# Optimization experiments

Hardware: AMD Instinct MI355X
Metric: run time of the kernel (lower is better)

The kernel has to match this reference:

```python
import jax, jax.numpy as jnp
import numpy as np

B, S, H, NH, BLK, R = 2, 4096, 768, 12, 64, 3
D = H // NH
NB = S // BLK
PENALTY = -10000.0


def setup_inputs() -> dict:
    key = jax.random.key(0)
    ks = jax.random.split(key, 5)
    return {
        "hidden_states": jax.random.normal(ks[0], (B, S, H), dtype=jnp.float32),
        "Wq": jax.random.normal(ks[1], (H, H), dtype=jnp.float32) * 0.02,
        "Wk": jax.random.normal(ks[2], (H, H), dtype=jnp.float32) * 0.02,
        "Wv": jax.random.normal(ks[3], (H, H), dtype=jnp.float32) * 0.02,
        "band_mask": jnp.ones((B, 1, NB - 4, BLK, 3 * BLK), dtype=jnp.float32),
        "from_mask": jnp.ones((B, 1, S, 1), dtype=jnp.float32),
        "to_mask": jnp.ones((B, 1, 1, S), dtype=jnp.float32),
        "from_blocked_mask": jnp.ones((B, NB, BLK), dtype=jnp.float32),
        "to_blocked_mask": jnp.ones((B, NB, BLK), dtype=jnp.float32),
        "rand_attn": jax.random.randint(ks[4], (B, NH, NB - 2, R), 0, NB, dtype=jnp.int64),
    }


def reference(hidden_states, Wq, Wk, Wv, band_mask, from_mask, to_mask,
              from_blocked_mask, to_blocked_mask, rand_attn):
    b, s, _ = hidden_states.shape
    nb, blk, r = NB, BLK, R
    rsqrt_d = 1.0 / jnp.sqrt(jnp.float32(D))
    sm = jax.nn.softmax

    # projections -> [b, h, s, d]
    def proj(W):
        return jnp.einsum('bse,ed->bsd', hidden_states, W).reshape(b, s, NH, D).transpose(0, 2, 1, 3)
    q, k, v = proj(Wq), proj(Wk), proj(Wv)

    bq = q.reshape(b, NH, nb, blk, D)
    bk = k.reshape(b, NH, nb, blk, D)
    bv = v.reshape(b, NH, nb, blk, D)

    # gather random key/value blocks: [b, h, nb-2, r*blk, d]
    bi = jnp.arange(b)[:, None, None, None]
    hi = jnp.arange(NH)[None, :, None, None]
    gk = bk[bi, hi, rand_attn].reshape(b, NH, nb - 2, r * blk, D)
    gv = bv[bi, hi, rand_attn].reshape(b, NH, nb - 2, r * blk, D)

    # random mask: [b, h, nb-2, blk, r*blk]
    rm = to_blocked_mask[jnp.arange(b)[:, None, None, None], rand_attn]  # [b,h,nb-2,r,blk]
    rm = rm.reshape(b, NH, nb - 2, r * blk)
    rand_mask = jnp.einsum('blq,bhlk->bhlqk', from_blocked_mask[:, 1:-1], rm)

    ones_rand = jnp.ones((b, 1, 1, r * blk), dtype=to_mask.dtype)
    ones_4blk = jnp.ones((b, NH, blk, 4 * blk), dtype=rand_mask.dtype)

    # --- first (global) block: attends to everything ---
    fp = jnp.einsum('bhqd,bhkd->bhqk', bq[:, :, 0], k) * rsqrt_d + (1.0 - to_mask) * PENALTY
    fc = jnp.einsum('bhqk,bhkd->bhqd', sm(fp, axis=-1), v)[:, :, None]  # [b,h,1,blk,d]

    # --- second block: first 3 blocks + last block + random blocks ---
    sk = jnp.concatenate([bk[:, :, 0], bk[:, :, 1], bk[:, :, 2], bk[:, :, -1], gk[:, :, 0]], axis=2)
    sv = jnp.concatenate([bv[:, :, 0], bv[:, :, 1], bv[:, :, 2], bv[:, :, -1], gv[:, :, 0]], axis=2)
    sp = jnp.einsum('bhqd,bhkd->bhqk', bq[:, :, 1], sk) * rsqrt_d
    seq_pad = jnp.concatenate([to_mask[:, :, :, :3 * blk], to_mask[:, :, :, -blk:], ones_rand], axis=3)
    rand_pad = jnp.concatenate([ones_4blk, rand_mask[:, :, 0]], axis=3)
    sp = sp + (1.0 - jnp.minimum(seq_pad, rand_pad)) * PENALTY
    sc = jnp.einsum('bhqk,bhkd->bhqd', sm(sp, axis=-1), sv)[:, :, None]

    # --- middle blocks: sliding window + global first/last + random ---
    ek = jnp.concatenate([bk[:, :, 1:-3], bk[:, :, 2:-2], bk[:, :, 3:-1]], axis=3)  # [b,h,nb-4,3blk,d]
    ev = jnp.concatenate([bv[:, :, 1:-3], bv[:, :, 2:-2], bv[:, :, 3:-1]], axis=3)
    mq = bq[:, :, 2:-2]
    inner = jnp.einsum('bhlqd,bhlkd->bhlqk', mq, ek) * rsqrt_d + (1.0 - band_mask) * PENALTY
    randb = jnp.einsum('bhlqd,bhlkd->bhlqk', mq, gk[:, :, 1:-1]) * rsqrt_d + (1.0 - rand_mask[:, :, 1:-1]) * PENALTY
    firstb = jnp.einsum('bhlqd,bhkd->bhlqk', mq, bk[:, :, 0]) * rsqrt_d + (1.0 - to_mask[:, :, :, None, :blk]) * PENALTY
    lastb = jnp.einsum('bhlqd,bhkd->bhlqk', mq, bk[:, :, -1]) * rsqrt_d + (1.0 - to_mask[:, :, :, None, -blk:]) * PENALTY
    band = jnp.concatenate([firstb, inner, randb, lastb], axis=-1)  # [...,(5+r)*blk]
    aw = sm(band, axis=-1)
    ctx_mid = (jnp.einsum('bhlqk,bhlkd->bhlqd', aw[..., blk:4 * blk], ev)
               + jnp.einsum('bhlqk,bhlkd->bhlqd', aw[..., 4 * blk:-blk], gv[:, :, 1:-1])
               + jnp.einsum('bhlqk,bhkd->bhlqd', aw[..., :blk], bv[:, :, 0])
               + jnp.einsum('bhlqk,bhkd->bhlqd', aw[..., -blk:], bv[:, :, -1]))

    # --- second-last block ---
    slk = jnp.concatenate([bk[:, :, 0], bk[:, :, -3], bk[:, :, -2], bk[:, :, -1], gk[:, :, -1]], axis=2)
    slv = jnp.concatenate([bv[:, :, 0], bv[:, :, -3], bv[:, :, -2], bv[:, :, -1], gv[:, :, -1]], axis=2)
    slp = jnp.einsum('bhqd,bhkd->bhqk', bq[:, :, -2], slk) * rsqrt_d
    sl_seq_pad = jnp.concatenate([to_mask[:, :, :, :blk], to_mask[:, :, :, -3 * blk:], ones_rand], axis=3)
    sl_rand_pad = jnp.concatenate([ones_4blk, rand_mask[:, :, -1]], axis=3)
    slp = slp + (1.0 - jnp.minimum(sl_seq_pad, sl_rand_pad)) * PENALTY
    slc = jnp.einsum('bhqk,bhkd->bhqd', sm(slp, axis=-1), slv)[:, :, None]

    # --- last (global) block ---
    lp = jnp.einsum('bhqd,bhkd->bhqk', bq[:, :, -1], k) * rsqrt_d + (1.0 - to_mask) * PENALTY
    lc = jnp.einsum('bhqk,bhkd->bhqd', sm(lp, axis=-1), v)[:, :, None]

    ctx = jnp.concatenate([fc, sc, ctx_mid, slc, lc], axis=2).reshape(b, NH, s, D)
    ctx = ctx * from_mask  # [b,1,s,1] broadcast
    return ctx.transpose(0, 2, 1, 3).reshape(b, s, NH * D)
```

## Files before the change

kernel.cpp:

```cpp
#include <hip/hip_runtime.h>
#include <hip/hip_bf16.h>
#include <stdint.h>

#define NHD 12
#define SLEN 4096
#define DH 64
#define NBLK 64
#define HDIM 768
#define PEN -10000.0f

typedef __bf16 bf16x8 __attribute__((ext_vector_type(8)));
typedef float f32x4 __attribute__((ext_vector_type(4)));
typedef unsigned short u16x8 __attribute__((ext_vector_type(8)));

__device__ __forceinline__ unsigned short f2bf(float x) {
    union { float f; unsigned u; } v; v.f = x;
    unsigned r = v.u + 0x7fffu + ((v.u >> 16) & 1u);
    return (unsigned short)(r >> 16);
}

__device__ __forceinline__ void gl2lds16(const void* g, void* l) {
    __builtin_amdgcn_global_load_lds(
        (const __attribute__((address_space(1))) void*)g,
        (__attribute__((address_space(3))) void*)l, 16, 0, 0);
}

__global__ void k_cast_hs(const float* __restrict__ in, unsigned short* __restrict__ out, int n8) {
    int i = blockIdx.x * blockDim.x + threadIdx.x;
    if (i >= n8) return;
    const float4* p = (const float4*)in + (size_t)i * 2;
    float4 a = p[0], b = p[1];
    u16x8 o;
    o[0]=f2bf(a.x); o[1]=f2bf(a.y); o[2]=f2bf(a.z); o[3]=f2bf(a.w);
    o[4]=f2bf(b.x); o[5]=f2bf(b.y); o[6]=f2bf(b.z); o[7]=f2bf(b.w);
    ((u16x8*)out)[i] = o;
}

__global__ void k_wt(const float* __restrict__ Wq, const float* __restrict__ Wk,
                     const float* __restrict__ Wv, unsigned short* __restrict__ wt) {
    const float* W = blockIdx.z == 0 ? Wq : (blockIdx.z == 1 ? Wk : Wv);
    unsigned short* out = wt + (size_t)blockIdx.z * HDIM * HDIM;
    __shared__ float tile[64][65];
    int t = threadIdx.x;
    int k0 = blockIdx.x * 64, n0 = blockIdx.y * 64;
    int r = t >> 2, c4 = t & 3;
#pragma unroll
    for (int j = 0; j < 16; j += 4) {
        float4 v = *(const float4*)&W[(size_t)(k0 + r) * HDIM + n0 + c4 * 16 + j];
        tile[r][c4*16+j+0] = v.x; tile[r][c4*16+j+1] = v.y;
        tile[r][c4*16+j+2] = v.z; tile[r][c4*16+j+3] = v.w;
    }
    __syncthreads();
    u16x8 o0, o1;
#pragma unroll
    for (int j = 0; j < 8; ++j) o0[j] = f2bf(tile[c4*16 + j][r]);
#pragma unroll
    for (int j = 0; j < 8; ++j) o1[j] = f2bf(tile[c4*16 + 8 + j][r]);
    *(u16x8*)&out[(size_t)(n0 + r) * HDIM + k0 + c4*16]     = o0;
    *(u16x8*)&out[(size_t)(n0 + r) * HDIM + k0 + c4*16 + 8] = o1;
}

__global__ __launch_bounds__(256) void k_proj(const unsigned short* __restrict__ hsb,
                                              const unsigned short* __restrict__ wtb,
                                              unsigned short* __restrict__ qkv) {
    __shared__ unsigned short As[128][72];
    __shared__ unsigned short Bs[128][72];
    const unsigned short* Bw = wtb + (size_t)blockIdx.z * HDIM * HDIM;
    unsigned short* out = qkv + (size_t)blockIdx.z * (2u * NHD * SLEN * DH);
    int m0 = blockIdx.x * 128, n0 = blockIdx.y * 128;
    int t = threadIdx.x;
    int w = t >> 6, l = t & 63, g = l >> 4, c = l & 15;
    int wm = w >> 1, wn = w & 1;
    int sr = t >> 1, sh = (t & 1) * 32;
    f32x4 acc[4][4];
#pragma unroll
    for (int i = 0; i < 4; ++i)
#pragma unroll
        for (int j = 0; j < 4; ++j) acc[i][j] = (f32x4){0.f,0.f,0.f,0.f};

    for (int kt = 0; kt < HDIM; kt += 64) {
        __syncthreads();
#pragma unroll
        for (int j = 0; j < 4; ++j) {
            *(u16x8*)&As[sr][sh + 8*j] = *(const u16x8*)&hsb[(size_t)(m0 + sr) * HDIM + kt + sh + 8*j];
            *(u16x8*)&Bs[sr][sh + 8*j] = *(const u16x8*)&Bw[(size_t)(n0 + sr) * HDIM + kt + sh + 8*j];
        }
        __syncthreads();
#pragma unroll
        for (int ks = 0; ks < 2; ++ks) {
            bf16x8 af[4], bf_[4];
#pragma unroll
            for (int mt = 0; mt < 4; ++mt) af[mt]  = *(const bf16x8*)&As[64*wm + 16*mt + c][32*ks + 8*g];
#pragma unroll
            for (int nt = 0; nt < 4; ++nt) bf_[nt] = *(const bf16x8*)&Bs[64*wn + 16*nt + c][32*ks + 8*g];
#pragma unroll
            for (int mt = 0; mt < 4; ++mt)
#pragma unroll
                for (int nt = 0; nt < 4; ++nt)
                    acc[mt][nt] = __builtin_amdgcn_mfma_f32_16x16x32_bf16(af[mt], bf_[nt], acc[mt][nt], 0, 0, 0);
        }
    }
#pragma unroll
    for (int mt = 0; mt < 4; ++mt)
#pragma unroll
        for (int nt = 0; nt < 4; ++nt)
#pragma unroll
            for (int r2 = 0; r2 < 4; ++r2) {
                int m = m0 + 64*wm + 16*mt + 4*g + r2;
                int n = n0 + 64*wn + 16*nt + c;
                int bb = m >> 12, s = m & 4095;
                int hh = n >> 6,  d = n & 63;
                out[(((size_t)bb * NHD + hh) * SLEN + s) * DH + d] = f2bf(acc[mt][nt][r2]);
            }
}

__global__ void k_vtrans(const unsigned short* __restrict__ v, unsigned short* __restrict__ vt) {
    __shared__ unsigned tile[64][65];
    int bh = blockIdx.y;
    int s0 = blockIdx.x * 64;
    int t = threadIdx.x;
    int r = t >> 2, c4 = t & 3;
    const unsigned short* vb = v + (size_t)bh * SLEN * DH;
#pragma unroll
    for (int jj = 0; jj < 16; jj += 8) {
        u16x8 x = *(const u16x8*)&vb[(size_t)(s0 + r) * DH + c4*16 + jj];
#pragma unroll
        for (int e = 0; e < 8; ++e) tile[r][c4*16 + jj + e] = x[e];
    }
    __syncthreads();
    unsigned short* vto = vt + (size_t)bh * DH * SLEN;
    int d = t >> 2;
    u16x8 o0, o1;
#pragma unroll
    for (int j = 0; j < 8; ++j) o0[j] = (unsigned short)tile[c4*16 + j][d];
#pragma unroll
    for (int j = 0; j < 8; ++j) o1[j] = (unsigned short)tile[c4*16 + 8 + j][d];
    *(u16x8*)&vto[(size_t)d * SLEN + s0 + c4*16]     = o0;
    *(u16x8*)&vto[(size_t)d * SLEN + s0 + c4*16 + 8] = o1;
}

__global__ __launch_bounds__(256) void k_attn(
    const unsigned short* __restrict__ Qb, const unsigned short* __restrict__ Kb,
    const unsigned short* __restrict__ VTb,
    const int* __restrict__ rand_attn,
    const float* __restrict__ band_mask, const float* __restrict__ from_mask,
    const float* __restrict__ to_mask, const float* __restrict__ fbm,
    const float* __restrict__ tbm,
    float* __restrict__ out, float* __restrict__ partials)
{
    __shared__ __align__(16) unsigned short Kt[2][4096];
    __shared__ __align__(16) unsigned short Vt[2][4096];
    __shared__ __align__(16) char plds[4 * 2048];

    int i0 = blockIdx.x;
    int gid = (i0 & 7) * 234 + (i0 >> 3);
    int bh = gid / 78, task = gid - bh * 78;
    int b = bh / NHD, h = bh - b * NHD;
    int t = threadIdx.x;
    int wq = t >> 6, l = t & 63, g = l >> 4, c = l & 15;
    int lr = l >> 3, ls = l & 7, sw = ls ^ lr;

    int row, mode = 0, pslot = 0;
    int blkj[8], kvj[8], sbj[8];
#pragma unroll
    for (int j = 0; j < 8; ++j) sbj[j] = 0;
    if (task < 8) {
        row = 0; mode = 1; pslot = task;
#pragma unroll
        for (int j = 0; j < 8; ++j) { blkj[j] = task * 8 + j; kvj[j] = 0; }
    } else if (task >= 70) {
        row = 63; mode = 1; pslot = task - 70;
#pragma unroll
        for (int j = 0; j < 8; ++j) { blkj[j] = pslot * 8 + j; kvj[j] = 0; }
    } else {
        row = task - 7;
        int rbase = ((b * NHD + h) * 62 + (row - 1)) * 3;
        blkj[4] = rand_attn[rbase];
        blkj[5] = rand_attn[rbase + 1];
        blkj[6] = rand_attn[rbase + 2];
        kvj[4] = kvj[5] = kvj[6] = 2;
        blkj[0] = 0; kvj[0] = 0;
        if (row == 1) {
            blkj[1]=1;  blkj[2]=2;  blkj[3]=63; kvj[1]=kvj[2]=kvj[3]=0;
            blkj[7]=0;  kvj[7]=3;
        } else if (row == 62) {
            blkj[1]=61; blkj[2]=62; blkj[3]=63; kvj[1]=kvj[2]=kvj[3]=0;
            blkj[7]=0;  kvj[7]=3;
        } else {
            blkj[1]=row-1; blkj[2]=row; blkj[3]=row+1;
            kvj[1]=kvj[2]=kvj[3]=1; sbj[1]=0; sbj[2]=64; sbj[3]=128;
            blkj[7]=63; kvj[7]=0;
        }
    }

    size_t bhoff = (size_t)bh * SLEN * DH;
    const char* Kbase = (const char*)(Kb + bhoff);
    const char* Vbase = (const char*)(VTb + (size_t)bh * DH * SLEN);
    int q0 = row * 64 + wq * 16;

    bf16x8 qf[2];
#pragma unroll
    for (int kk = 0; kk < 2; ++kk)
        qf[kk] = *(const bf16x8*)&Qb[bhoff + (size_t)(q0 + c) * DH + kk * 32 + 8 * g];

    float fmq = fbm[(b * NBLK + row) * 64 + wq * 16 + c];
    size_t bm_base = ((size_t)(b * 60 + row - 2) * 64 + (wq * 16 + c)) * 192;
    int tm_base = b * SLEN;

    float m_run = -1e30f, l_run = 0.f;
    f32x4 o_acc[4];
#pragma unroll
    for (int dt = 0; dt < 4; ++dt) o_acc[dt] = (f32x4){0.f,0.f,0.f,0.f};

    char* myl = plds + wq * 2048 + c * 128;
    int swz = (c & 7) << 4;

    auto stage = [&](int blk, int nb) __attribute__((always_inline)) {
#pragma unroll
        for (int ii = 0; ii < 2; ++ii) {
            int i = wq * 2 + ii;
            const char* ksrc = Kbase + (size_t)blk * 8192 + (size_t)(i*8 + lr) * 128 + sw * 16;
            gl2lds16(ksrc, (char*)&Kt[nb][0] + i * 1024);
            const char* vsrc = Vbase + (size_t)(i*8 + lr) * 8192 + (size_t)blk * 128 + sw * 16;
            gl2lds16(vsrc, (char*)&Vt[nb][0] + i * 1024);
        }
    };

    auto loadmask = [&](int kv, int blk, int sb, float4* mk) __attribute__((always_inline)) {
        if (kv == 0) {
#pragma unroll
            for (int mt = 0; mt < 4; ++mt)
                mk[mt] = *(const float4*)&to_mask[tm_base + blk * 64 + mt * 16 + 4 * g];
        } else if (kv == 1) {
#pragma unroll
            for (int mt = 0; mt < 4; ++mt)
                mk[mt] = *(const float4*)&band_mask[bm_base + sb + mt * 16 + 4 * g];
        } else if (kv == 2) {
#pragma unroll
            for (int mt = 0; mt < 4; ++mt)
                mk[mt] = *(const float4*)&tbm[(size_t)(b * NBLK + blk) * 64 + mt * 16 + 4 * g];
        }
    };

    auto compute = [&](int kv, int nb, const float4* mk) __attribute__((always_inline)) {
        if (kv == 3) return;
        int c7 = c & 7;
        bf16x8 kf[4][2];
#pragma unroll
        for (int mt = 0; mt < 4; ++mt)
#pragma unroll
            for (int kk = 0; kk < 2; ++kk)
                kf[mt][kk] = *(const bf16x8*)((const char*)&Kt[nb][0]
                              + (mt*16 + c) * 128 + (((kk*4 + g) ^ c7) * 16));

        f32x4 sa[4];
#pragma unroll
        for (int mt = 0; mt < 4; ++mt) sa[mt] = (f32x4){0.f,0.f,0.f,0.f};
#pragma unroll
        for (int kk = 0; kk < 2; ++kk)
#pragma unroll
            for (int mt = 0; mt < 4; ++mt)
                sa[mt] = __builtin_amdgcn_mfma_f32_16x16x32_bf16(kf[mt][kk], qf[kk], sa[mt], 0, 0, 0);

        float fmk = (kv == 2) ? fmq : 1.f;
#pragma unroll
        for (int mt = 0; mt < 4; ++mt) {
            sa[mt][0] = sa[mt][0] * 0.125f + (1.f - fmk * mk[mt].x) * PEN;
            sa[mt][1] = sa[mt][1] * 0.125f + (1.f - fmk * mk[mt].y) * PEN;
            sa[mt][2] = sa[mt][2] * 0.125f + (1.f - fmk * mk[mt].z) * PEN;
            sa[mt][3] = sa[mt][3] * 0.125f + (1.f - fmk * mk[mt].w) * PEN;
        }

        float pm = -1e30f;
#pragma unroll
        for (int mt = 0; mt < 4; ++mt)
#pragma unroll
            for (int r2 = 0; r2 < 4; ++r2) pm = fmaxf(pm, sa[mt][r2]);
        pm = fmaxf(pm, __shfl_xor(pm, 16));
        pm = fmaxf(pm, __shfl_xor(pm, 32));
        bool need = pm > m_run + 8.f;
        float mnew = need ? pm : m_run;
        float scale = __expf(m_run - mnew);
        m_run = mnew;
        l_run *= scale;
#pragma unroll
        for (int dt = 0; dt < 4; ++dt)
#pragma unroll
            for (int r2 = 0; r2 < 4; ++r2) o_acc[dt][r2] *= scale;

        float rs = 0.f;
#pragma unroll
        for (int mt = 0; mt < 4; ++mt)
#pragma unroll
            for (int r2 = 0; r2 < 4; ++r2) {
                float e = __expf(sa[mt][r2] - m_run);
                sa[mt][r2] = e;
                rs += e;
            }
        rs += __shfl_xor(rs, 16);
        rs += __shfl_xor(rs, 32);
        l_run += rs;

#pragma unroll
        for (int mt = 0; mt < 4; ++mt) {
            unsigned lo = (unsigned)f2bf(sa[mt][0]) | ((unsigned)f2bf(sa[mt][1]) << 16);
            unsigned hi = (unsigned)f2bf(sa[mt][2]) | ((unsigned)f2bf(sa[mt][3]) << 16);
            unsigned long long pk = (unsigned long long)lo | ((unsigned long long)hi << 32);
            *(unsigned long long*)(myl + ((mt * 32 + g * 8) ^ swz)) = pk;
        }
        asm volatile("" ::: "memory");
        bf16x8 pf0 = *(const bf16x8*)(myl + ((g * 16) ^ swz));
        bf16x8 pf1 = *(const bf16x8*)(myl + ((64 + g * 16) ^ swz));

#pragma unroll
        for (int dt = 0; dt < 4; ++dt) {
            bf16x8 v0 = *(const bf16x8*)((const char*)&Vt[nb][0]
                          + (dt*16 + c) * 128 + ((g ^ c7) * 16));
            bf16x8 v1 = *(const bf16x8*)((const char*)&Vt[nb][0]
                          + (dt*16 + c) * 128 + (((4 + g) ^ c7) * 16));
            o_acc[dt] = __builtin_amdgcn_mfma_f32_16x16x32_bf16(v0, pf0, o_acc[dt], 0, 0, 0);
            o_acc[dt] = __builtin_amdgcn_mfma_f32_16x16x32_bf16(v1, pf1, o_acc[dt], 0, 0, 0);
        }
    };

    float4 mkA[4], mkB[4];
    stage(blkj[0], 0);
    loadmask(kvj[0], blkj[0], sbj[0], mkA);
    __syncthreads();
#pragma unroll
    for (int tt = 0; tt < 8; ++tt) {
        if (tt < 7) {
            stage(blkj[tt + 1], (tt & 1) ^ 1);
            loadmask(kvj[tt + 1], blkj[tt + 1], sbj[tt + 1], (tt & 1) ? mkA : mkB);
        }
        compute(kvj[tt], tt & 1, (tt & 1) ? mkB : mkA);
        __syncthreads();
    }

    if (mode == 0) {
        int s = q0 + c;
        float fm = from_mask[b * SLEN + s];
        float inv = fm / l_run;
        size_t obase = ((size_t)b * SLEN + s) * HDIM + h * DH;
#pragma unroll
        for (int dt = 0; dt < 4; ++dt) {
            float4 val;
            val.x = o_acc[dt][0] * inv;
            val.y = o_acc[dt][1] * inv;
            val.z = o_acc[dt][2] * inv;
            val.w = o_acc[dt][3] * inv;
            *(float4*)&out[obase + dt * 16 + 4 * g] = val;
        }
    } else {
        float* pb = partials + (size_t)((bh * 2 + (row == 63 ? 1 : 0)) * 8 + pslot) * 4224;
        int q = wq * 16 + c;
#pragma unroll
        for (int dt = 0; dt < 4; ++dt) {
            float4 val;
            val.x = o_acc[dt][0]; val.y = o_acc[dt][1];
            val.z = o_acc[dt][2]; val.w = o_acc[dt][3];
            *(float4*)&pb[q * 64 + dt * 16 + 4 * g] = val;
        }
        if (g == 0) {
            pb[4096 + q] = m_run;
            pb[4160 + q] = l_run;
        }
    }
}

__global__ void k_combine(const float* __restrict__ partials, const float* __restrict__ from_mask,
                          float* __restrict__ out) {
    int gid = blockIdx.x;
    int bh = gid >> 1, rb = gid & 1;
    int b = bh / NHD, h = bh - b * NHD;
    int t = threadIdx.x;
    int q = t >> 2, dc = (t & 3) * 16;
    const float* base = partials + (size_t)gid * 8 * 4224;
    float M = -1e30f;
#pragma unroll
    for (int i = 0; i < 8; ++i) M = fmaxf(M, base[i*4224 + 4096 + q]);
    float L = 0.f, cx[16];
#pragma unroll
    for (int j = 0; j < 16; ++j) cx[j] = 0.f;
    for (int i = 0; i < 8; ++i) {
        float w = __expf(base[i*4224 + 4096 + q] - M);
        L += base[i*4224 + 4160 + q] * w;
#pragma unroll
        for (int j = 0; j < 16; ++j) cx[j] += base[i*4224 + q*64 + dc + j] * w;
    }
    int s = (rb ? 4032 : 0) + q;
    float fm = from_mask[b * SLEN + s];
    float inv = fm / L;
#pragma unroll
    for (int j = 0; j < 16; ++j)
        out[((size_t)b * SLEN + s) * HDIM + h * DH + dc + j] = cx[j] * inv;
}

extern "C" void kernel_launch(void* const* d_in, const int* in_sizes, int n_in,
                              void* d_out, int out_size, void* d_ws, size_t ws_size,
                              hipStream_t stream) {
    const float* hs    = (const float*)d_in[0];
    const float* Wq    = (const float*)d_in[1];
    const float* Wk    = (const float*)d_in[2];
    const float* Wv    = (const float*)d_in[3];
    const float* band  = (const float*)d_in[4];
    const float* fromm = (const float*)d_in[5];
    const float* tom   = (const float*)d_in[6];
    const float* fbm   = (const float*)d_in[7];
    const float* tbm   = (const float*)d_in[8];
    const int*   ra    = (const int*)d_in[9];
    float* out = (float*)d_out;

    char* ws = (char*)d_ws;
    unsigned short* hsb = (unsigned short*)(ws);
    unsigned short* vtb = (unsigned short*)(ws);
    unsigned short* wtb = (unsigned short*)(ws + 12582912);
    unsigned short* qkv = (unsigned short*)(ws + 16121856);
    float* partials     = (float*)(ws + 53870592);

    k_cast_hs<<<3072, 256, 0, stream>>>(hs, hsb, 786432);
    k_wt<<<dim3(12, 12, 3), 256, 0, stream>>>(Wq, Wk, Wv, wtb);
    k_proj<<<dim3(64, 6, 3), 256, 0, stream>>>(hsb, wtb, qkv);
    k_vtrans<<<dim3(64, 24), 256, 0, stream>>>(qkv + 2 * 6291456, vtb);
    k_attn<<<1872, 256, 0, stream>>>(qkv, qkv + 6291456, vtb, ra,
                                     band, fromm, tom, fbm, tbm, out, partials);
    k_combine<<<48, 256, 0, stream>>>(partials, fromm, out);
}
```

Measured before the change: 117.9 us.

## Fuse V transpose into projection, use async LDS loads, exp2 softmax with skip

The projection GEMM now loads tiles straight into swizzled LDS with global_load_lds. A transposed variant writes V directly in [d][s] layout, which removes the separate vtrans kernel and its round trip through memory. Attention folds log2e into the scale and precomputes the mask penalties during prefetch. It uses exp2f and skips the output rescale when no lane's running max changes, and converts to bf16 with native casts. The extra launch and the transposed scattered stores add cost in exchange.

```diff
diff --git a/kernel.cpp b/kernel.cpp
--- a/kernel.cpp
+++ b/kernel.cpp
@@ -8,6 +8,7 @@
 #define NBLK 64
 #define HDIM 768
 #define PEN -10000.0f
+#define LOG2E 1.44269504f
 
 typedef __bf16 bf16x8 __attribute__((ext_vector_type(8)));
 typedef float f32x4 __attribute__((ext_vector_type(4)));
@@ -60,18 +61,21 @@
     *(u16x8*)&out[(size_t)(n0 + r) * HDIM + k0 + c4*16 + 8] = o1;
 }
 
+template<bool TR>
 __global__ __launch_bounds__(256) void k_proj(const unsigned short* __restrict__ hsb,
                                               const unsigned short* __restrict__ wtb,
-                                              unsigned short* __restrict__ qkv) {
-    __shared__ unsigned short As[128][72];
-    __shared__ unsigned short Bs[128][72];
-    const unsigned short* Bw = wtb + (size_t)blockIdx.z * HDIM * HDIM;
-    unsigned short* out = qkv + (size_t)blockIdx.z * (2u * NHD * SLEN * DH);
+                                              unsigned short* __restrict__ outbuf) {
+    __shared__ __align__(16) unsigned short As[8192];
+    __shared__ __align__(16) unsigned short Bs[8192];
+    const char* Abase = (const char*)hsb;
+    const char* Bbase = (const char*)(wtb + (size_t)blockIdx.z * HDIM * HDIM);
+    unsigned short* out = outbuf + (size_t)blockIdx.z * (2u * NHD * SLEN * DH);
     int m0 = blockIdx.x * 128, n0 = blockIdx.y * 128;
     int t = threadIdx.x;
     int w = t >> 6, l = t & 63, g = l >> 4, c = l & 15;
     int wm = w >> 1, wn = w & 1;
-    int sr = t >> 1, sh = (t & 1) * 32;
+    int lr = l >> 3, ls = l & 7, sw = ls ^ lr;
+    int c7 = c & 7;
     f32x4 acc[4][4];
 #pragma unroll
     for (int i = 0; i < 4; ++i)
@@ -81,62 +85,54 @@
     for (int kt = 0; kt < HDIM; kt += 64) {
         __syncthreads();
 #pragma unroll
-        for (int j = 0; j < 4; ++j) {
-            *(u16x8*)&As[sr][sh + 8*j] = *(const u16x8*)&hsb[(size_t)(m0 + sr) * HDIM + kt + sh + 8*j];
-            *(u16x8*)&Bs[sr][sh + 8*j] = *(const u16x8*)&Bw[(size_t)(n0 + sr) * HDIM + kt + sh + 8*j];
+        for (int i = 0; i < 4; ++i) {
+            int rowb = w * 32 + i * 8;
+            gl2lds16(Abase + (size_t)(m0 + rowb + lr) * 1536 + kt * 2 + sw * 16,
+                     (char*)As + rowb * 128);
+            gl2lds16(Bbase + (size_t)(n0 + rowb + lr) * 1536 + kt * 2 + sw * 16,
+                     (char*)Bs + rowb * 128);
         }
         __syncthreads();
 #pragma unroll
         for (int ks = 0; ks < 2; ++ks) {
             bf16x8 af[4], bf_[4];
 #pragma unroll
-            for (int mt = 0; mt < 4; ++mt) af[mt]  = *(const bf16x8*)&As[64*wm + 16*mt + c][32*ks + 8*g];
-#pragma unroll
-            for (int nt = 0; nt < 4; ++nt) bf_[nt] = *(const bf16x8*)&Bs[64*wn + 16*nt + c][32*ks + 8*g];
-#pragma unroll
             for (int mt = 0; mt < 4; ++mt)
-#pragma unroll
-                for (int nt = 0; nt < 4; ++nt)
-                    acc[mt][nt] = __builtin_amdgcn_mfma_f32_16x16x32_bf16(af[mt], bf_[nt], acc[mt][nt], 0, 0, 0);
-        }
-    }
-#pragma unroll
-    for (int mt = 0; mt < 4; ++mt)
-#pragma unroll
-        for (int nt = 0; nt < 4; ++nt)
+                af[mt]  = *(const bf16x8*)((const char*)As
+                            + (64*wm + 16*mt + c) * 128 + (((ks*4 + g) ^ c7) * 16));
+#pragma unroll
+            for (int nt = 0; nt < 4; ++nt)
+                bf_[nt] = *(const bf16x8*)((const char*)Bs
+                            + (64*wn + 16*nt + c) * 128 + (((ks*4 + g) ^ c7) * 16));
+#pragma unroll
+            for (int i = 0; i < 4; ++i)
+#pragma unroll
+                for (int j = 0; j < 4; ++j)
+                    acc[i][j] = TR
+                        ? __builtin_amdgcn_mfma_f32_16x16x32_bf16(bf_[i], af[j], acc[i][j], 0, 0, 0)
+                        : __builtin_amdgcn_mfma_f32_16x16x32_bf16(af[i], bf_[j], acc[i][j], 0, 0, 0);
+        }
+    }
+#pragma unroll
+    for (int i = 0; i < 4; ++i)
+#pragma unroll
+        for (int j = 0; j < 4; ++j)
 #pragma unroll
             for (int r2 = 0; r2 < 4; ++r2) {
-                int m = m0 + 64*wm + 16*mt + 4*g + r2;
-                int n = n0 + 64*wn + 16*nt + c;
-                int bb = m >> 12, s = m & 4095;
-                int hh = n >> 6,  d = n & 63;
-                out[(((size_t)bb * NHD + hh) * SLEN + s) * DH + d] = f2bf(acc[mt][nt][r2]);
+                if (!TR) {
+                    int m = m0 + 64*wm + 16*i + 4*g + r2;
+                    int n = n0 + 64*wn + 16*j + c;
+                    int bb = m >> 12, s = m & 4095;
+                    int hh = n >> 6,  d = n & 63;
+                    out[(((size_t)bb * NHD + hh) * SLEN + s) * DH + d] = f2bf(acc[i][j][r2]);
+                } else {
+                    int n = n0 + 64*wn + 16*i + 4*g + r2;
+                    int m = m0 + 64*wm + 16*j + c;
+                    int bb = m >> 12, s = m & 4095;
+                    int hh = n >> 6,  d = n & 63;
+                    out[(((size_t)bb * NHD + hh) * DH + d) * SLEN + s] = f2bf(acc[i][j][r2]);
+                }
             }
-}
-
-__global__ void k_vtrans(const unsigned short* __restrict__ v, unsigned short* __restrict__ vt) {
-    __shared__ unsigned tile[64][65];
-    int bh = blockIdx.y;
-    int s0 = blockIdx.x * 64;
-    int t = threadIdx.x;
-    int r = t >> 2, c4 = t & 3;
-    const unsigned short* vb = v + (size_t)bh * SLEN * DH;
-#pragma unroll
-    for (int jj = 0; jj < 16; jj += 8) {
-        u16x8 x = *(const u16x8*)&vb[(size_t)(s0 + r) * DH + c4*16 + jj];
-#pragma unroll
-        for (int e = 0; e < 8; ++e) tile[r][c4*16 + jj + e] = x[e];
-    }
-    __syncthreads();
-    unsigned short* vto = vt + (size_t)bh * DH * SLEN;
-    int d = t >> 2;
-    u16x8 o0, o1;
-#pragma unroll
-    for (int j = 0; j < 8; ++j) o0[j] = (unsigned short)tile[c4*16 + j][d];
-#pragma unroll
-    for (int j = 0; j < 8; ++j) o1[j] = (unsigned short)tile[c4*16 + 8 + j][d];
-    *(u16x8*)&vto[(size_t)d * SLEN + s0 + c4*16]     = o0;
-    *(u16x8*)&vto[(size_t)d * SLEN + s0 + c4*16 + 8] = o1;
 }
 
 __global__ __launch_bounds__(256) void k_attn(
@@ -151,6 +147,10 @@
     __shared__ __align__(16) unsigned short Kt[2][4096];
     __shared__ __align__(16) unsigned short Vt[2][4096];
     __shared__ __align__(16) char plds[4 * 2048];
+
+    const float SC = 0.125f * LOG2E;
+    const float PL = PEN * LOG2E;
+    const float THR2 = 8.0f * LOG2E;
 
     int i0 = blockIdx.x;
     int gid = (i0 & 7) * 234 + (i0 >> 3);
@@ -226,23 +226,32 @@
         }
     };
 
-    auto loadmask = [&](int kv, int blk, int sb, float4* mk) __attribute__((always_inline)) {
+    auto loadpen = [&](int kv, int blk, int sb, float4* pen) __attribute__((always_inline)) {
         if (kv == 0) {
 #pragma unroll
-            for (int mt = 0; mt < 4; ++mt)
-                mk[mt] = *(const float4*)&to_mask[tm_base + blk * 64 + mt * 16 + 4 * g];
+            for (int mt = 0; mt < 4; ++mt) {
+                float4 mk = *(const float4*)&to_mask[tm_base + blk * 64 + mt * 16 + 4 * g];
+                pen[mt].x = (1.f - mk.x) * PL; pen[mt].y = (1.f - mk.y) * PL;
+                pen[mt].z = (1.f - mk.z) * PL; pen[mt].w = (1.f - mk.w) * PL;
+            }
         } else if (kv == 1) {
 #pragma unroll
-            for (int mt = 0; mt < 4; ++mt)
-                mk[mt] = *(const float4*)&band_mask[bm_base + sb + mt * 16 + 4 * g];
+            for (int mt = 0; mt < 4; ++mt) {
+                float4 mk = *(const float4*)&band_mask[bm_base + sb + mt * 16 + 4 * g];
+                pen[mt].x = (1.f - mk.x) * PL; pen[mt].y = (1.f - mk.y) * PL;
+                pen[mt].z = (1.f - mk.z) * PL; pen[mt].w = (1.f - mk.w) * PL;
+            }
         } else if (kv == 2) {
 #pragma unroll
-            for (int mt = 0; mt < 4; ++mt)
-                mk[mt] = *(const float4*)&tbm[(size_t)(b * NBLK + blk) * 64 + mt * 16 + 4 * g];
+            for (int mt = 0; mt < 4; ++mt) {
+                float4 tb = *(const float4*)&tbm[(size_t)(b * NBLK + blk) * 64 + mt * 16 + 4 * g];
+                pen[mt].x = (1.f - fmq * tb.x) * PL; pen[mt].y = (1.f - fmq * tb.y) * PL;
+                pen[mt].z = (1.f - fmq * tb.z) * PL; pen[mt].w = (1.f - fmq * tb.w) * PL;
+            }
         }
     };
 
-    auto compute = [&](int kv, int nb, const float4* mk) __attribute__((always_inline)) {
+    auto compute = [&](int kv, int nb, const float4* pen) __attribute__((always_inline)) {
         if (kv == 3) return;
         int c7 = c & 7;
         bf16x8 kf[4][2];
@@ -262,13 +271,12 @@
             for (int mt = 0; mt < 4; ++mt)
                 sa[mt] = __builtin_amdgcn_mfma_f32_16x16x32_bf16(kf[mt][kk], qf[kk], sa[mt], 0, 0, 0);
 
-        float fmk = (kv == 2) ? fmq : 1.f;
 #pragma unroll
         for (int mt = 0; mt < 4; ++mt) {
-            sa[mt][0] = sa[mt][0] * 0.125f + (1.f - fmk * mk[mt].x) * PEN;
-            sa[mt][1] = sa[mt][1] * 0.125f + (1.f - fmk * mk[mt].y) * PEN;
-            sa[mt][2] = sa[mt][2] * 0.125f + (1.f - fmk * mk[mt].z) * PEN;
-            sa[mt][3] = sa[mt][3] * 0.125f + (1.f - fmk * mk[mt].w) * PEN;
+            sa[mt][0] = sa[mt][0] * SC + pen[mt].x;
+            sa[mt][1] = sa[mt][1] * SC + pen[mt].y;
+            sa[mt][2] = sa[mt][2] * SC + pen[mt].z;
+            sa[mt][3] = sa[mt][3] * SC + pen[mt].w;
         }
 
         float pm = -1e30f;
@@ -278,22 +286,24 @@
             for (int r2 = 0; r2 < 4; ++r2) pm = fmaxf(pm, sa[mt][r2]);
         pm = fmaxf(pm, __shfl_xor(pm, 16));
         pm = fmaxf(pm, __shfl_xor(pm, 32));
-        bool need = pm > m_run + 8.f;
-        float mnew = need ? pm : m_run;
-        float scale = __expf(m_run - mnew);
-        m_run = mnew;
-        l_run *= scale;
-#pragma unroll
-        for (int dt = 0; dt < 4; ++dt)
-#pragma unroll
-            for (int r2 = 0; r2 < 4; ++r2) o_acc[dt][r2] *= scale;
+        if (__ballot(pm > m_run + THR2)) {
+            bool need = pm > m_run + THR2;
+            float mnew = need ? pm : m_run;
+            float scale = exp2f(m_run - mnew);
+            m_run = mnew;
+            l_run *= scale;
+#pragma unroll
+            for (int dt = 0; dt < 4; ++dt)
+#pragma unroll
+                for (int r2 = 0; r2 < 4; ++r2) o_acc[dt][r2] *= scale;
+        }
 
         float rs = 0.f;
 #pragma unroll
         for (int mt = 0; mt < 4; ++mt)
 #pragma unroll
             for (int r2 = 0; r2 < 4; ++r2) {
-                float e = __expf(sa[mt][r2] - m_run);
+                float e = exp2f(sa[mt][r2] - m_run);
                 sa[mt][r2] = e;
                 rs += e;
             }
@@ -303,10 +313,10 @@
 
 #pragma unroll
         for (int mt = 0; mt < 4; ++mt) {
-            unsigned lo = (unsigned)f2bf(sa[mt][0]) | ((unsigned)f2bf(sa[mt][1]) << 16);
-            unsigned hi = (unsigned)f2bf(sa[mt][2]) | ((unsigned)f2bf(sa[mt][3]) << 16);
-            unsigned long long pk = (unsigned long long)lo | ((unsigned long long)hi << 32);
-            *(unsigned long long*)(myl + ((mt * 32 + g * 8) ^ swz)) = pk;
+            union { __bf16 hh[4]; unsigned long long u; } pk_;
+            pk_.hh[0] = (__bf16)sa[mt][0]; pk_.hh[1] = (__bf16)sa[mt][1];
+            pk_.hh[2] = (__bf16)sa[mt][2]; pk_.hh[3] = (__bf16)sa[mt][3];
+            *(unsigned long long*)(myl + ((mt * 32 + g * 8) ^ swz)) = pk_.u;
         }
         asm volatile("" ::: "memory");
         bf16x8 pf0 = *(const bf16x8*)(myl + ((g * 16) ^ swz));
@@ -323,17 +333,17 @@
         }
     };
 
-    float4 mkA[4], mkB[4];
+    float4 penA[4], penB[4];
     stage(blkj[0], 0);
-    loadmask(kvj[0], blkj[0], sbj[0], mkA);
+    loadpen(kvj[0], blkj[0], sbj[0], penA);
     __syncthreads();
 #pragma unroll
     for (int tt = 0; tt < 8; ++tt) {
         if (tt < 7) {
             stage(blkj[tt + 1], (tt & 1) ^ 1);
-            loadmask(kvj[tt + 1], blkj[tt + 1], sbj[tt + 1], (tt & 1) ? mkA : mkB);
-        }
-        compute(kvj[tt], tt & 1, (tt & 1) ? mkB : mkA);
+            loadpen(kvj[tt + 1], blkj[tt + 1], sbj[tt + 1], (tt & 1) ? penA : penB);
+        }
+        compute(kvj[tt], tt & 1, (tt & 1) ? penB : penA);
         __syncthreads();
     }
 
@@ -383,7 +393,7 @@
 #pragma unroll
     for (int j = 0; j < 16; ++j) cx[j] = 0.f;
     for (int i = 0; i < 8; ++i) {
-        float w = __expf(base[i*4224 + 4096 + q] - M);
+        float w = exp2f(base[i*4224 + 4096 + q] - M);
         L += base[i*4224 + 4160 + q] * w;
 #pragma unroll
         for (int j = 0; j < 16; ++j) cx[j] += base[i*4224 + q*64 + dc + j] * w;
@@ -413,16 +423,16 @@
 
     char* ws = (char*)d_ws;
     unsigned short* hsb = (unsigned short*)(ws);
-    unsigned short* vtb = (unsigned short*)(ws);
     unsigned short* wtb = (unsigned short*)(ws + 12582912);
     unsigned short* qkv = (unsigned short*)(ws + 16121856);
     float* partials     = (float*)(ws + 53870592);
 
     k_cast_hs<<<3072, 256, 0, stream>>>(hs, hsb, 786432);
     k_wt<<<dim3(12, 12, 3), 256, 0, stream>>>(Wq, Wk, Wv, wtb);
-    k_proj<<<dim3(64, 6, 3), 256, 0, stream>>>(hsb, wtb, qkv);
-    k_vtrans<<<dim3(64, 24), 256, 0, stream>>>(qkv + 2 * 6291456, vtb);
-    k_attn<<<1872, 256, 0, stream>>>(qkv, qkv + 6291456, vtb, ra,
+    k_proj<false><<<dim3(64, 6, 2), 256, 0, stream>>>(hsb, wtb, qkv);
+    k_proj<true><<<dim3(64, 6, 1), 256, 0, stream>>>(hsb, wtb + 2 * HDIM * HDIM,
+                                                     qkv + 2 * 6291456);
+    k_attn<<<1872, 256, 0, stream>>>(qkv, qkv + 6291456, qkv + 2 * 6291456, ra,
                                      band, fromm, tom, fbm, tbm, out, partials);
     k_combine<<<48, 256, 0, stream>>>(partials, fromm, out);
 }
```

Measured after the change: 109.7 us. 7.0% less time.
